# Kernel optimization log

Hardware: AMD Instinct MI355X
Metric: run time of the kernel (lower is better)

Reference implementation:

```python
import jax, jax.numpy as jnp
import numpy as np

B, S, DM = 2, 2048, 1024
H, D = 16, 64  # multiheads, head_dim; H*D == DM
NEG = -1e9


def setup_inputs() -> dict:
    key = jax.random.key(0)
    ks = jax.random.split(key, 7)
    xavier = float(np.sqrt(6.0 / (DM + H * D)))
    return {
        "Q": jax.random.normal(ks[0], (B, S, DM), dtype=jnp.float32),
        "K": jax.random.normal(ks[1], (B, S, DM), dtype=jnp.float32),
        "V": jax.random.normal(ks[2], (B, S, DM), dtype=jnp.float32),
        "V_len": jax.random.randint(ks[3], (B,), 0, S),
        "WQ": jax.random.uniform(ks[4], (DM, H * D), dtype=jnp.float32, minval=-xavier, maxval=xavier),
        "WK": jax.random.uniform(ks[5], (DM, H * D), dtype=jnp.float32, minval=-xavier, maxval=xavier),
        "WV": jax.random.uniform(ks[6], (DM, H * D), dtype=jnp.float32, minval=-xavier, maxval=xavier),
    }


def reference(Q, K, V, V_len, WQ, WK, WV):
    b, s, _ = Q.shape
    # project and split heads: [B,S,DM] -> [B,H,S,D]
    q = (Q @ WQ).reshape(b, s, H, D).transpose(0, 2, 1, 3)
    k = (K @ WK).reshape(b, s, H, D).transpose(0, 2, 1, 3)
    v = (V @ WV).reshape(b, s, H, D).transpose(0, 2, 1, 3)
    scores = jnp.einsum("bhqd,bhkd->bhqk", q, k) / jnp.sqrt(jnp.float32(D))
    # key padding mask: valid keys are positions < V_len[b]
    valid = jnp.arange(s)[None, :] < V_len[:, None]          # [B,S]
    scores = jnp.where(valid[:, None, None, :], scores, NEG)  # [B,H,Sq,Sk]
    attn = jax.nn.softmax(scores, axis=-1)
    out = jnp.einsum("bhqk,bhkd->bhqd", attn, v)
    return out.transpose(0, 2, 1, 3).reshape(b, s, H * D)
```

## Files before the change

kernel.cpp:

```cpp
#include <hip/hip_runtime.h>
#include <hip/hip_bf16.h>

#define NBATCH 2
#define SEQ 2048
#define DMODEL 1024
#define NHEAD 16
#define HDIM 64
#define ROWS (NBATCH*SEQ)

typedef __attribute__((ext_vector_type(8))) short bf16x8;
typedef __attribute__((ext_vector_type(4))) float f32x4;
typedef __attribute__((ext_vector_type(16))) float f32x16;

#define MFMA16 __builtin_amdgcn_mfma_f32_16x16x32_bf16
#define MFMA32 __builtin_amdgcn_mfma_f32_32x32x16_bf16

#define QSCALE 0.1803368801111204f
#define DEFER_THR 11.541560327111708f

static __device__ __forceinline__ unsigned short f2bf(float f) {
    unsigned int u = __float_as_uint(f);
    u += 0x7fffu + ((u >> 16) & 1u);
    return (unsigned short)(u >> 16);
}

static __device__ __forceinline__ unsigned cvtpk(float lo, float hi) {
    unsigned r;
    asm("v_cvt_pk_bf16_f32 %0, %1, %2" : "=v"(r) : "v"(lo), "v"(hi));
    return r;
}

static __device__ __forceinline__ void gld16(const unsigned short* g, unsigned short* l) {
    __builtin_amdgcn_global_load_lds(
        (const __attribute__((address_space(1))) unsigned int*)g,
        (__attribute__((address_space(3))) unsigned int*)l,
        16, 0, 0);
}

__global__ __launch_bounds__(256) void cvt_kernel(const float* __restrict__ Q, const float* __restrict__ K,
                                                  const float* __restrict__ V, const int* __restrict__ vlenp,
                                                  unsigned short* __restrict__ dq, unsigned short* __restrict__ dk,
                                                  unsigned short* __restrict__ dv, int n8) {
    int i = blockIdx.x * 256 + threadIdx.x;
    if (i >= n8) return;
    const int z = blockIdx.z;
    if (z) {
        int row = i >> 7;
        int bb = row >> 11, s = row & 2047;
        int vl = vlenp[bb];
        int lim = ((vl + 31) >> 5) << 5;
        if (z == 1) { if (vl == 0 || s >= lim) return; }
        else        { if (vl != 0 && s >= lim) return; }
    }
    const float* src = z == 0 ? Q : (z == 1 ? K : V);
    unsigned short* dst = z == 0 ? dq : (z == 1 ? dk : dv);
    const float4* s4 = (const float4*)src;
    float4 a = s4[2 * i], b = s4[2 * i + 1];
    union { bf16x8 v; unsigned short u[8]; } o;
    o.u[0] = f2bf(a.x); o.u[1] = f2bf(a.y); o.u[2] = f2bf(a.z); o.u[3] = f2bf(a.w);
    o.u[4] = f2bf(b.x); o.u[5] = f2bf(b.y); o.u[6] = f2bf(b.z); o.u[7] = f2bf(b.w);
    *(bf16x8*)(dst + (size_t)i * 8) = o.v;
}

__global__ __launch_bounds__(256) void wtrans_kernel(const float* __restrict__ W0, const float* __restrict__ W1,
                                                     const float* __restrict__ W2,
                                                     unsigned short* __restrict__ T0, unsigned short* __restrict__ T1,
                                                     unsigned short* __restrict__ T2) {
    const float* W = blockIdx.z == 0 ? W0 : (blockIdx.z == 1 ? W1 : W2);
    unsigned short* T = blockIdx.z == 0 ? T0 : (blockIdx.z == 1 ? T1 : T2);
    __shared__ float tile[64][65];
    int rb = blockIdx.y * 64, cb = blockIdx.x * 64;
    int tid = threadIdx.x;
    #pragma unroll
    for (int rep = 0; rep < 16; ++rep) {
        int idx = rep * 256 + tid; int r = idx >> 6, c = idx & 63;
        tile[r][c] = W[(size_t)(rb + r) * DMODEL + cb + c];
    }
    __syncthreads();
    #pragma unroll
    for (int rep = 0; rep < 16; ++rep) {
        int idx = rep * 256 + tid; int r = idx >> 6, c = idx & 63;
        T[(size_t)(cb + r) * DMODEL + rb + c] = f2bf(tile[c][r]);
    }
}

__global__ __launch_bounds__(256) void proj_kernel(
        const unsigned short* __restrict__ Xq, const unsigned short* __restrict__ Xk,
        const unsigned short* __restrict__ Xv,
        const unsigned short* __restrict__ WTq, const unsigned short* __restrict__ WTk,
        const unsigned short* __restrict__ WTv, const int* __restrict__ vlenp,
        unsigned short* __restrict__ qp, unsigned short* __restrict__ kp,
        unsigned short* __restrict__ vtp) {
    const int mode = blockIdx.z;
    {
    }
    const int lin = blockIdx.y * gridDim.x + blockIdx.x;
    const int xcd = lin & 7, chunk = lin >> 3;
    const int by2 = xcd * 4 + (chunk >> 3);
    const int bx2 = chunk & 7;
    const int rowBase = by2 * 128;
    const int colBase = bx2 * 128;

    if (mode >= 1) {
        const int bb = rowBase >> 11, sS = rowBase & 2047;
        const int vl = vlenp[bb];
        const int lim = ((vl + 31) >> 5) << 5;
        if (mode == 1) { if (vl == 0 || sS >= lim) return; }
        else           { if (vl != 0 && sS >= lim) return; }
    }

    const unsigned short* X  = mode == 0 ? Xq  : (mode == 1 ? Xk  : Xv);
    const unsigned short* WT = mode == 0 ? WTq : (mode == 1 ? WTk : WTv);

    __shared__ unsigned short As[2][128 * 64];
    __shared__ unsigned short Bs[2][128 * 64];

    const int tid = threadIdx.x, lane = tid & 63, w = tid >> 6;
    const int wr = w >> 1, wc = w & 1;

    const int Xwave = (mode < 2) ? wr : wc;
    const int Wwave = (mode < 2) ? wc : wr;

    const int rloc = lane >> 3;
    const int ssw  = ((lane & 7) * 8) ^ (rloc * 8);

    f32x4 acc[4][4];
    #pragma unroll
    for (int i = 0; i < 4; ++i)
        #pragma unroll
        for (int j = 0; j < 4; ++j) acc[i][j] = (f32x4){0.f, 0.f, 0.f, 0.f};

    auto stage = [&](int kt, int buf) {
        #pragma unroll
        for (int j = 0; j < 4; ++j) {
            int c = w * 4 + j;
            int r = c * 8 + rloc;
            gld16(X  + (size_t)(rowBase + r) * DMODEL + kt * 64 + ssw, &As[buf][c * 512]);
            gld16(WT + (size_t)(colBase + r) * DMODEL + kt * 64 + ssw, &Bs[buf][c * 512]);
        }
    };

    stage(0, 0);
    __syncthreads();

    for (int kt = 0; kt < DMODEL / 64; ++kt) {
        const int cur = kt & 1;
        if (kt + 1 < DMODEL / 64) stage(kt + 1, cur ^ 1);

        #pragma unroll
        for (int ks = 0; ks < 2; ++ks) {
            const int kbyte = ks * 64 + ((lane >> 4) * 16);
            bf16x8 xf[4], wf[4];
            #pragma unroll
            for (int i = 0; i < 4; ++i) {
                int xr = Xwave * 64 + i * 16 + (lane & 15);
                xf[i] = *(const bf16x8*)((const char*)&As[cur][0] + xr * 128 + (kbyte ^ ((xr & 7) << 4)));
                int wrow = Wwave * 64 + i * 16 + (lane & 15);
                wf[i] = *(const bf16x8*)((const char*)&Bs[cur][0] + wrow * 128 + (kbyte ^ ((wrow & 7) << 4)));
            }
            if (mode < 2) {
                #pragma unroll
                for (int i = 0; i < 4; ++i)
                    #pragma unroll
                    for (int j = 0; j < 4; ++j)
                        acc[i][j] = MFMA16(xf[i], wf[j], acc[i][j], 0, 0, 0);
            } else {
                #pragma unroll
                for (int i = 0; i < 4; ++i)
                    #pragma unroll
                    for (int j = 0; j < 4; ++j)
                        acc[i][j] = MFMA16(wf[i], xf[j], acc[i][j], 0, 0, 0);
            }
        }
        __syncthreads();
    }

    if (mode < 2) {
        unsigned short* outp = (mode == 0) ? qp : kp;
        const float sc = (mode == 0) ? QSCALE : 1.0f;
        #pragma unroll
        for (int i = 0; i < 4; ++i)
            #pragma unroll
            for (int j = 0; j < 4; ++j)
                #pragma unroll
                for (int r = 0; r < 4; ++r) {
                    int grow = rowBase + wr * 64 + i * 16 + (lane >> 4) * 4 + r;
                    int gcol = colBase + wc * 64 + j * 16 + (lane & 15);
                    int b = grow >> 11, s = grow & 2047, hh = gcol >> 6, d = gcol & 63;
                    outp[((size_t)(b * NHEAD + hh) * SEQ + s) * HDIM + d] = f2bf(acc[i][j][r] * sc);
                }
    } else {
        #pragma unroll
        for (int i = 0; i < 4; ++i)
            #pragma unroll
            for (int j = 0; j < 4; ++j)
                #pragma unroll
                for (int r = 0; r < 4; ++r) {
                    int gcol = colBase + wr * 64 + i * 16 + (lane >> 4) * 4 + r;
                    int grow = rowBase + wc * 64 + j * 16 + (lane & 15);
                    int b = grow >> 11, s = grow & 2047, hh = gcol >> 6, d = gcol & 63;
                    vtp[((size_t)(b * NHEAD + hh) * HDIM + d) * SEQ + s] = f2bf(acc[i][j][r]);
                }
    }
}

__global__ __launch_bounds__(256, 4) void attn_kernel(
        const unsigned short* __restrict__ qp, const unsigned short* __restrict__ kp,
        const unsigned short* __restrict__ vtp, const int* __restrict__ vlenp,
        float* __restrict__ out) {
    const int tid = threadIdx.x, lane = tid & 63, w = tid >> 6;
    const int hh = lane >> 5;
    const int ql = lane & 31;
    const int qsub = w >> 1, kpar = w & 1;
    const int qt = blockIdx.x, h = blockIdx.y, b = blockIdx.z;
    const int vlen = vlenp[b];
    const int nt = (vlen == 0) ? (SEQ / 32) : ((vlen + 31) >> 5);
    const int myn = (nt - kpar + 1) >> 1;
    const int J = (nt + 1) >> 1;

    __shared__ unsigned short Kd[2][2][2048];
    __shared__ unsigned short Vd[2][2][2048];
    __shared__ float mlb[4][2][32];

    const size_t headQ = (size_t)(b * NHEAD + h) * SEQ * HDIM;
    const size_t headV = (size_t)(b * NHEAD + h) * HDIM * SEQ;

    const int qrow = qt * 64 + qsub * 32 + ql;
    bf16x8 qf[4];
    #pragma unroll
    for (int ks = 0; ks < 4; ++ks)
        qf[ks] = *(const bf16x8*)(qp + headQ + (size_t)qrow * HDIM + ks * 16 + hh * 8);

    f32x16 o0, o1;
    #pragma unroll
    for (int r = 0; r < 16; ++r) { o0[r] = 0.f; o1[r] = 0.f; }
    float m_run = -1e30f, l_run = 0.f;

    const int rloc = lane >> 3;
    const int ssw  = ((lane & 7) * 8) ^ (rloc * 8);
    const int gn   = (lane & 7) ^ rloc;
    const int koff = (gn & 3) * 8;
    const int dhi  = (gn >> 2) * 32;

    auto stageK = [&](int kvB, int buf) {
        #pragma unroll
        for (int c = 0; c < 4; ++c)
            gld16(kp + headQ + (size_t)(kvB + c * 8 + rloc) * HDIM + ssw, &Kd[kpar][buf][c * 512]);
    };
    auto stageV = [&](int kvB, int buf) {
        #pragma unroll
        for (int c = 0; c < 4; ++c)
            gld16(vtp + headV + (size_t)(c * 8 + rloc + dhi) * SEQ + kvB + koff, &Vd[kpar][buf][c * 512]);
    };

    if (myn > 0) { if (qsub == 0) stageK(kpar * 32, 0); else stageV(kpar * 32, 0); }

    for (int j = 0; j < J; ++j) {
        const int cur = j & 1;
        __syncthreads();

        if (j + 1 < myn) {
            const int nb = (kpar + 2 * (j + 1)) * 32;
            if (qsub == 0) stageK(nb, cur ^ 1); else stageV(nb, cur ^ 1);
        }

        if (j < myn) {
            const int kvBase = (kpar + 2 * j) * 32;
            const char* Kb = (const char*)&Kd[kpar][cur][0];
            const char* Vb = (const char*)&Vd[kpar][cur][0];

            f32x16 s0;
            #pragma unroll
            for (int r = 0; r < 16; ++r) s0[r] = 0.f;
            __builtin_amdgcn_s_setprio(1);
            #pragma unroll
            for (int ks = 0; ks < 4; ++ks) {
                const int kb = (ks * 32 + hh * 16) ^ ((ql & 7) << 4);
                bf16x8 kf = *(const bf16x8*)(Kb + ql * 128 + kb);
                s0 = MFMA32(kf, qf[ks], s0, 0, 0, 0);
            }
            __builtin_amdgcn_s_setprio(0);

            if (kvBase + 32 > vlen) {
                #pragma unroll
                for (int r = 0; r < 16; ++r) {
                    int kl = (r & 3) + 8 * (r >> 2) + 4 * hh;
                    if (kvBase + kl >= vlen) s0[r] = -1e9f;
                }
            }

            float mx[8];
            #pragma unroll
            for (int t = 0; t < 8; ++t) mx[t] = fmaxf(s0[t], s0[t + 8]);
            #pragma unroll
            for (int st = 4; st > 0; st >>= 1)
                #pragma unroll
                for (int t = 0; t < st; ++t) mx[t] = fmaxf(mx[t], mx[t + st]);
            float tmax = fmaxf(mx[0], __shfl_xor(mx[0], 32));

            if (!__all(tmax <= m_run + DEFER_THR)) {
                const float mnew = fmaxf(m_run, tmax);
                const float al = __builtin_amdgcn_exp2f(m_run - mnew);
                l_run *= al;
                #pragma unroll
                for (int r = 0; r < 16; ++r) { o0[r] *= al; o1[r] *= al; }
                m_run = mnew;
            }

            #pragma unroll
            for (int r = 0; r < 16; ++r) s0[r] = __builtin_amdgcn_exp2f(s0[r] - m_run);
            float sm[8];
            #pragma unroll
            for (int t = 0; t < 8; ++t) sm[t] = s0[t] + s0[t + 8];
            #pragma unroll
            for (int st = 4; st > 0; st >>= 1)
                #pragma unroll
                for (int t = 0; t < st; ++t) sm[t] += sm[t + st];
            l_run += sm[0] + __shfl_xor(sm[0], 32);

            unsigned d0[8];
            #pragma unroll
            for (int t = 0; t < 8; ++t) d0[t] = cvtpk(s0[2 * t], s0[2 * t + 1]);

            __builtin_amdgcn_s_setprio(1);
#define PV_SLICE(KSL)                                                              \
            {                                                                      \
                unsigned a0 = d0[4 * (KSL)],     b0 = d0[4 * (KSL) + 2];           \
                unsigned a1 = d0[4 * (KSL) + 1], b1 = d0[4 * (KSL) + 3];           \
                asm("v_permlane32_swap_b32 %0, %1" : "+v"(a0), "+v"(b0));          \
                asm("v_permlane32_swap_b32 %0, %1" : "+v"(a1), "+v"(b1));          \
                union { unsigned u[4]; bf16x8 v; } pa;                             \
                pa.u[0] = a0; pa.u[1] = a1; pa.u[2] = b0; pa.u[3] = b1;            \
                const int gA = 2 * (KSL) + hh;                                     \
                bf16x8 vfA = *(const bf16x8*)(Vb + ql * 128 + ((gA ^ (ql & 7)) << 4));        \
                bf16x8 vfB = *(const bf16x8*)(Vb + ql * 128 + (((4 + gA) ^ (ql & 7)) << 4));  \
                o0 = MFMA32(vfA, pa.v, o0, 0, 0, 0);                               \
                o1 = MFMA32(vfB, pa.v, o1, 0, 0, 0);                               \
            }
            PV_SLICE(0)
            PV_SLICE(1)
#undef PV_SLICE
            __builtin_amdgcn_s_setprio(0);
        }
    }

    if (hh == 0) { mlb[w][0][ql] = m_run; mlb[w][1][ql] = l_run; }
    __syncthreads();
    if (kpar == 1) {
        char* Ob = ((char*)Kd) + qsub * 8192;
        #pragma unroll
        for (int g = 0; g < 4; ++g) {
            int ad = ql * 256 + ((32 * g + 16 * hh) ^ (16 * (ql & 7)));
            *(float4*)(Ob + ad)       = make_float4(o0[4*g], o0[4*g+1], o0[4*g+2], o0[4*g+3]);
            *(float4*)(Ob + ad + 128) = make_float4(o1[4*g], o1[4*g+1], o1[4*g+2], o1[4*g+3]);
        }
    }
    __syncthreads();
    if (kpar == 0) {
        const float mp = mlb[w + 1][0][ql], lp = mlb[w + 1][1][ql];
        const float M = fmaxf(m_run, mp);
        const float a0 = __builtin_amdgcn_exp2f(m_run - M);
        const float a1 = __builtin_amdgcn_exp2f(mp - M);
        const float linv = 1.0f / (l_run * a0 + lp * a1);
        const char* Pb = ((const char*)Kd) + qsub * 8192;
        float* orow = out + (size_t)(b * SEQ + qrow) * DMODEL + h * HDIM;
        #pragma unroll
        for (int g = 0; g < 4; ++g) {
            int ad = ql * 256 + ((32 * g + 16 * hh) ^ (16 * (ql & 7)));
            float4 p0 = *(const float4*)(Pb + ad);
            float4 p1 = *(const float4*)(Pb + ad + 128);
            *(float4*)(orow + 8 * g + 4 * hh) = make_float4(
                (o0[4*g]   * a0 + p0.x * a1) * linv, (o0[4*g+1] * a0 + p0.y * a1) * linv,
                (o0[4*g+2] * a0 + p0.z * a1) * linv, (o0[4*g+3] * a0 + p0.w * a1) * linv);
            *(float4*)(orow + 32 + 8 * g + 4 * hh) = make_float4(
                (o1[4*g]   * a0 + p1.x * a1) * linv, (o1[4*g+1] * a0 + p1.y * a1) * linv,
                (o1[4*g+2] * a0 + p1.z * a1) * linv, (o1[4*g+3] * a0 + p1.w * a1) * linv);
        }
    }
}

extern "C" void kernel_launch(void* const* d_in, const int* in_sizes, int n_in,
                              void* d_out, int out_size, void* d_ws, size_t ws_size,
                              hipStream_t stream) {
    const float* Q  = (const float*)d_in[0];
    const float* K  = (const float*)d_in[1];
    const float* V  = (const float*)d_in[2];
    const int* V_len = (const int*)d_in[3];
    const float* WQ = (const float*)d_in[4];
    const float* WK = (const float*)d_in[5];
    const float* WV = (const float*)d_in[6];
    float* out = (float*)d_out;

    char* ws = (char*)d_ws;
    const size_t MB = 1024 * 1024;
    unsigned short* Xq  = (unsigned short*)(ws + 0 * MB);
    unsigned short* Xk  = (unsigned short*)(ws + 8 * MB);
    unsigned short* Xv  = (unsigned short*)(ws + 16 * MB);
    unsigned short* WTq = (unsigned short*)(ws + 24 * MB);
    unsigned short* WTk = (unsigned short*)(ws + 26 * MB);
    unsigned short* WTv = (unsigned short*)(ws + 28 * MB);
    unsigned short* qpj = (unsigned short*)(ws + 30 * MB);
    unsigned short* kpj = (unsigned short*)(ws + 38 * MB);
    unsigned short* vtp = (unsigned short*)(ws + 46 * MB);

    const int n8 = ROWS * DMODEL / 8;
    cvt_kernel<<<dim3((n8 + 255) / 256, 1, 3), 256, 0, stream>>>(Q, K, V, V_len, Xq, Xk, Xv, n8);
    wtrans_kernel<<<dim3(16, 16, 3), 256, 0, stream>>>(WQ, WK, WV, WTq, WTk, WTv);
    proj_kernel<<<dim3(8, 32, 3), 256, 0, stream>>>(
        Xq, Xk, Xv, WTq, WTk, WTv, V_len, qpj, kpj, vtp);
    attn_kernel<<<dim3(SEQ / 64, NHEAD, NBATCH), 256, 0, stream>>>(qpj, kpj, vtp, V_len, out);
}
```

Before: 88.09 us.

## Fold weight transpose into convert kernel and use single-buffered 128-wide K tiles

The weight transpose/convert kernel is merged into the input convert kernel as an extra grid z-slice, which removes one kernel launch. The projection GEMM drops its double-buffered 64-wide K staging. It now loads 128-wide K tiles into a single LDS buffer, with a barrier before compute, so the main loop runs half as many iterations and barriers. The trade-off is that global-to-LDS loads no longer overlap MFMA compute, which may expose memory latency in the projection.

```diff
diff --git a/kernel.cpp b/kernel.cpp
--- a/kernel.cpp
+++ b/kernel.cpp
@@ -39,11 +39,37 @@
 
 __global__ __launch_bounds__(256) void cvt_kernel(const float* __restrict__ Q, const float* __restrict__ K,
                                                   const float* __restrict__ V, const int* __restrict__ vlenp,
+                                                  const float* __restrict__ W0, const float* __restrict__ W1,
+                                                  const float* __restrict__ W2,
                                                   unsigned short* __restrict__ dq, unsigned short* __restrict__ dk,
-                                                  unsigned short* __restrict__ dv, int n8) {
-    int i = blockIdx.x * 256 + threadIdx.x;
+                                                  unsigned short* __restrict__ dv,
+                                                  unsigned short* __restrict__ T0, unsigned short* __restrict__ T1,
+                                                  unsigned short* __restrict__ T2, int n8) {
+    __shared__ float tile[64][65];
+    const int z = blockIdx.z;
+    const int tid = threadIdx.x;
+    if (z == 3) {
+        const int bx = blockIdx.x;
+        if (bx >= 768) return;
+        const int mat = bx >> 8, idx = bx & 255;
+        const float* W = mat == 0 ? W0 : (mat == 1 ? W1 : W2);
+        unsigned short* T = mat == 0 ? T0 : (mat == 1 ? T1 : T2);
+        int rb = (idx >> 4) * 64, cb = (idx & 15) * 64;
+        #pragma unroll
+        for (int rep = 0; rep < 16; ++rep) {
+            int i = rep * 256 + tid; int r = i >> 6, c = i & 63;
+            tile[r][c] = W[(size_t)(rb + r) * DMODEL + cb + c];
+        }
+        __syncthreads();
+        #pragma unroll
+        for (int rep = 0; rep < 16; ++rep) {
+            int i = rep * 256 + tid; int r = i >> 6, c = i & 63;
+            T[(size_t)(cb + r) * DMODEL + rb + c] = f2bf(tile[c][r]);
+        }
+        return;
+    }
+    int i = blockIdx.x * 256 + tid;
     if (i >= n8) return;
-    const int z = blockIdx.z;
     if (z) {
         int row = i >> 7;
         int bb = row >> 11, s = row & 2047;
@@ -62,28 +88,6 @@
     *(bf16x8*)(dst + (size_t)i * 8) = o.v;
 }
 
-__global__ __launch_bounds__(256) void wtrans_kernel(const float* __restrict__ W0, const float* __restrict__ W1,
-                                                     const float* __restrict__ W2,
-                                                     unsigned short* __restrict__ T0, unsigned short* __restrict__ T1,
-                                                     unsigned short* __restrict__ T2) {
-    const float* W = blockIdx.z == 0 ? W0 : (blockIdx.z == 1 ? W1 : W2);
-    unsigned short* T = blockIdx.z == 0 ? T0 : (blockIdx.z == 1 ? T1 : T2);
-    __shared__ float tile[64][65];
-    int rb = blockIdx.y * 64, cb = blockIdx.x * 64;
-    int tid = threadIdx.x;
-    #pragma unroll
-    for (int rep = 0; rep < 16; ++rep) {
-        int idx = rep * 256 + tid; int r = idx >> 6, c = idx & 63;
-        tile[r][c] = W[(size_t)(rb + r) * DMODEL + cb + c];
-    }
-    __syncthreads();
-    #pragma unroll
-    for (int rep = 0; rep < 16; ++rep) {
-        int idx = rep * 256 + tid; int r = idx >> 6, c = idx & 63;
-        T[(size_t)(cb + r) * DMODEL + rb + c] = f2bf(tile[c][r]);
-    }
-}
-
 __global__ __launch_bounds__(256) void proj_kernel(
         const unsigned short* __restrict__ Xq, const unsigned short* __restrict__ Xk,
         const unsigned short* __restrict__ Xv,
@@ -92,8 +96,6 @@
         unsigned short* __restrict__ qp, unsigned short* __restrict__ kp,
         unsigned short* __restrict__ vtp) {
     const int mode = blockIdx.z;
-    {
-    }
     const int lin = blockIdx.y * gridDim.x + blockIdx.x;
     const int xcd = lin & 7, chunk = lin >> 3;
     const int by2 = xcd * 4 + (chunk >> 3);
@@ -112,17 +114,14 @@
     const unsigned short* X  = mode == 0 ? Xq  : (mode == 1 ? Xk  : Xv);
     const unsigned short* WT = mode == 0 ? WTq : (mode == 1 ? WTk : WTv);
 
-    __shared__ unsigned short As[2][128 * 64];
-    __shared__ unsigned short Bs[2][128 * 64];
+    __shared__ unsigned short As[128 * 128];
+    __shared__ unsigned short Bs[128 * 128];
 
     const int tid = threadIdx.x, lane = tid & 63, w = tid >> 6;
     const int wr = w >> 1, wc = w & 1;
 
     const int Xwave = (mode < 2) ? wr : wc;
     const int Wwave = (mode < 2) ? wc : wr;
-
-    const int rloc = lane >> 3;
-    const int ssw  = ((lane & 7) * 8) ^ (rloc * 8);
 
     f32x4 acc[4][4];
     #pragma unroll
@@ -130,33 +129,29 @@
         #pragma unroll
         for (int j = 0; j < 4; ++j) acc[i][j] = (f32x4){0.f, 0.f, 0.f, 0.f};
 
-    auto stage = [&](int kt, int buf) {
-        #pragma unroll
-        for (int j = 0; j < 4; ++j) {
-            int c = w * 4 + j;
-            int r = c * 8 + rloc;
-            gld16(X  + (size_t)(rowBase + r) * DMODEL + kt * 64 + ssw, &As[buf][c * 512]);
-            gld16(WT + (size_t)(colBase + r) * DMODEL + kt * 64 + ssw, &Bs[buf][c * 512]);
-        }
-    };
-
-    stage(0, 0);
-    __syncthreads();
-
-    for (int kt = 0; kt < DMODEL / 64; ++kt) {
-        const int cur = kt & 1;
-        if (kt + 1 < DMODEL / 64) stage(kt + 1, cur ^ 1);
-
-        #pragma unroll
-        for (int ks = 0; ks < 2; ++ks) {
-            const int kbyte = ks * 64 + ((lane >> 4) * 16);
+    const int rl4 = lane >> 4;
+    const int gl  = lane & 15;
+
+    for (int kt = 0; kt < DMODEL / 128; ++kt) {
+        #pragma unroll
+        for (int j = 0; j < 8; ++j) {
+            int c = w * 8 + j;
+            int r = c * 4 + rl4;
+            int gg = gl ^ (r & 7);
+            gld16(X  + (size_t)(rowBase + r) * DMODEL + kt * 128 + gg * 8, &As[c * 512]);
+            gld16(WT + (size_t)(colBase + r) * DMODEL + kt * 128 + gg * 8, &Bs[c * 512]);
+        }
+        __syncthreads();
+        #pragma unroll
+        for (int ks = 0; ks < 4; ++ks) {
+            const int kbyteNom = ks * 64 + ((lane >> 4) * 16);
             bf16x8 xf[4], wf[4];
             #pragma unroll
             for (int i = 0; i < 4; ++i) {
                 int xr = Xwave * 64 + i * 16 + (lane & 15);
-                xf[i] = *(const bf16x8*)((const char*)&As[cur][0] + xr * 128 + (kbyte ^ ((xr & 7) << 4)));
+                xf[i] = *(const bf16x8*)((const char*)As + xr * 256 + (kbyteNom ^ ((xr & 7) << 4)));
                 int wrow = Wwave * 64 + i * 16 + (lane & 15);
-                wf[i] = *(const bf16x8*)((const char*)&Bs[cur][0] + wrow * 128 + (kbyte ^ ((wrow & 7) << 4)));
+                wf[i] = *(const bf16x8*)((const char*)Bs + wrow * 256 + (kbyteNom ^ ((wrow & 7) << 4)));
             }
             if (mode < 2) {
                 #pragma unroll
@@ -404,8 +399,8 @@
     unsigned short* vtp = (unsigned short*)(ws + 46 * MB);
 
     const int n8 = ROWS * DMODEL / 8;
-    cvt_kernel<<<dim3((n8 + 255) / 256, 1, 3), 256, 0, stream>>>(Q, K, V, V_len, Xq, Xk, Xv, n8);
-    wtrans_kernel<<<dim3(16, 16, 3), 256, 0, stream>>>(WQ, WK, WV, WTq, WTk, WTv);
+    cvt_kernel<<<dim3((n8 + 255) / 256, 1, 4), 256, 0, stream>>>(
+        Q, K, V, V_len, WQ, WK, WV, Xq, Xk, Xv, WTq, WTk, WTv, n8);
     proj_kernel<<<dim3(8, 32, 3), 256, 0, stream>>>(
         Xq, Xk, Xv, WTq, WTk, WTv, V_len, qpj, kpj, vtp);
     attn_kernel<<<dim3(SEQ / 64, NHEAD, NBATCH), 256, 0, stream>>>(qpj, kpj, vtp, V_len, out);
```

Measured after the change: 84.37 us. 4.2% less time.

## Fuse fp32-to-bf16 input conversion into projection GEMM and drop cvt kernel

Applied to the files above, without the earlier changes.

Removes the separate conversion kernel. The projection GEMM now loads fp32 activations directly, converts them to bf16 in registers and writes them swizzled into shared memory. This avoids a full write and re-read of bf16 copies of Q, K and V plus one launch. In exchange the K loop becomes single-buffered over 128-wide steps, losing the earlier async double-buffered prefetch, and it reads twice the bytes per activation tile. It also remaps the block-to-XCD row ordering and flattens the weight transpose grid.

```diff
diff --git a/kernel.cpp b/kernel.cpp
--- a/kernel.cpp
+++ b/kernel.cpp
@@ -37,66 +37,40 @@
         16, 0, 0);
 }
 
-__global__ __launch_bounds__(256) void cvt_kernel(const float* __restrict__ Q, const float* __restrict__ K,
-                                                  const float* __restrict__ V, const int* __restrict__ vlenp,
-                                                  unsigned short* __restrict__ dq, unsigned short* __restrict__ dk,
-                                                  unsigned short* __restrict__ dv, int n8) {
-    int i = blockIdx.x * 256 + threadIdx.x;
-    if (i >= n8) return;
-    const int z = blockIdx.z;
-    if (z) {
-        int row = i >> 7;
-        int bb = row >> 11, s = row & 2047;
-        int vl = vlenp[bb];
-        int lim = ((vl + 31) >> 5) << 5;
-        if (z == 1) { if (vl == 0 || s >= lim) return; }
-        else        { if (vl != 0 && s >= lim) return; }
-    }
-    const float* src = z == 0 ? Q : (z == 1 ? K : V);
-    unsigned short* dst = z == 0 ? dq : (z == 1 ? dk : dv);
-    const float4* s4 = (const float4*)src;
-    float4 a = s4[2 * i], b = s4[2 * i + 1];
-    union { bf16x8 v; unsigned short u[8]; } o;
-    o.u[0] = f2bf(a.x); o.u[1] = f2bf(a.y); o.u[2] = f2bf(a.z); o.u[3] = f2bf(a.w);
-    o.u[4] = f2bf(b.x); o.u[5] = f2bf(b.y); o.u[6] = f2bf(b.z); o.u[7] = f2bf(b.w);
-    *(bf16x8*)(dst + (size_t)i * 8) = o.v;
-}
-
 __global__ __launch_bounds__(256) void wtrans_kernel(const float* __restrict__ W0, const float* __restrict__ W1,
                                                      const float* __restrict__ W2,
                                                      unsigned short* __restrict__ T0, unsigned short* __restrict__ T1,
                                                      unsigned short* __restrict__ T2) {
-    const float* W = blockIdx.z == 0 ? W0 : (blockIdx.z == 1 ? W1 : W2);
-    unsigned short* T = blockIdx.z == 0 ? T0 : (blockIdx.z == 1 ? T1 : T2);
     __shared__ float tile[64][65];
-    int rb = blockIdx.y * 64, cb = blockIdx.x * 64;
-    int tid = threadIdx.x;
+    const int bx = blockIdx.x;
+    const int mat = bx >> 8, idx = bx & 255;
+    const float* W = mat == 0 ? W0 : (mat == 1 ? W1 : W2);
+    unsigned short* T = mat == 0 ? T0 : (mat == 1 ? T1 : T2);
+    const int rb = (idx >> 4) * 64, cb = (idx & 15) * 64;
+    const int tid = threadIdx.x;
     #pragma unroll
     for (int rep = 0; rep < 16; ++rep) {
-        int idx = rep * 256 + tid; int r = idx >> 6, c = idx & 63;
+        int i = rep * 256 + tid; int r = i >> 6, c = i & 63;
         tile[r][c] = W[(size_t)(rb + r) * DMODEL + cb + c];
     }
     __syncthreads();
     #pragma unroll
     for (int rep = 0; rep < 16; ++rep) {
-        int idx = rep * 256 + tid; int r = idx >> 6, c = idx & 63;
+        int i = rep * 256 + tid; int r = i >> 6, c = i & 63;
         T[(size_t)(cb + r) * DMODEL + rb + c] = f2bf(tile[c][r]);
     }
 }
 
 __global__ __launch_bounds__(256) void proj_kernel(
-        const unsigned short* __restrict__ Xq, const unsigned short* __restrict__ Xk,
-        const unsigned short* __restrict__ Xv,
+        const float* __restrict__ Xq, const float* __restrict__ Xk, const float* __restrict__ Xv,
         const unsigned short* __restrict__ WTq, const unsigned short* __restrict__ WTk,
         const unsigned short* __restrict__ WTv, const int* __restrict__ vlenp,
         unsigned short* __restrict__ qp, unsigned short* __restrict__ kp,
         unsigned short* __restrict__ vtp) {
     const int mode = blockIdx.z;
-    {
-    }
     const int lin = blockIdx.y * gridDim.x + blockIdx.x;
     const int xcd = lin & 7, chunk = lin >> 3;
-    const int by2 = xcd * 4 + (chunk >> 3);
+    const int by2 = (chunk >> 3) * 8 + xcd;
     const int bx2 = chunk & 7;
     const int rowBase = by2 * 128;
     const int colBase = bx2 * 128;
@@ -109,7 +83,7 @@
         else           { if (vl != 0 && sS >= lim) return; }
     }
 
-    const unsigned short* X  = mode == 0 ? Xq  : (mode == 1 ? Xk  : Xv);
+    const float* X = mode == 0 ? Xq : (mode == 1 ? Xk : Xv);
     const unsigned short* WT = mode == 0 ? WTq : (mode == 1 ? WTk : WTv);
 
     __shared__ unsigned short As[2][128 * 64];
@@ -117,12 +91,12 @@
 
     const int tid = threadIdx.x, lane = tid & 63, w = tid >> 6;
     const int wr = w >> 1, wc = w & 1;
-
     const int Xwave = (mode < 2) ? wr : wc;
     const int Wwave = (mode < 2) ? wc : wr;
 
     const int rloc = lane >> 3;
-    const int ssw  = ((lane & 7) * 8) ^ (rloc * 8);
+    const int gl8  = lane & 7;
+    const int ssw  = (gl8 * 8) ^ (rloc * 8);
 
     f32x4 acc[4][4];
     #pragma unroll
@@ -130,48 +104,58 @@
         #pragma unroll
         for (int j = 0; j < 4; ++j) acc[i][j] = (f32x4){0.f, 0.f, 0.f, 0.f};
 
-    auto stage = [&](int kt, int buf) {
+    for (int kt = 0; kt < DMODEL / 128; ++kt) {
+        #pragma unroll
+        for (int hf = 0; hf < 2; ++hf)
+            #pragma unroll
+            for (int j = 0; j < 4; ++j) {
+                int c = w * 4 + j;
+                int r = c * 8 + rloc;
+                gld16(WT + (size_t)(colBase + r) * DMODEL + kt * 128 + hf * 64 + ssw, &Bs[hf][c * 512]);
+            }
         #pragma unroll
         for (int j = 0; j < 4; ++j) {
-            int c = w * 4 + j;
-            int r = c * 8 + rloc;
-            gld16(X  + (size_t)(rowBase + r) * DMODEL + kt * 64 + ssw, &As[buf][c * 512]);
-            gld16(WT + (size_t)(colBase + r) * DMODEL + kt * 64 + ssw, &Bs[buf][c * 512]);
-        }
-    };
-
-    stage(0, 0);
-    __syncthreads();
-
-    for (int kt = 0; kt < DMODEL / 64; ++kt) {
-        const int cur = kt & 1;
-        if (kt + 1 < DMODEL / 64) stage(kt + 1, cur ^ 1);
-
-        #pragma unroll
-        for (int ks = 0; ks < 2; ++ks) {
-            const int kbyte = ks * 64 + ((lane >> 4) * 16);
-            bf16x8 xf[4], wf[4];
-            #pragma unroll
-            for (int i = 0; i < 4; ++i) {
-                int xr = Xwave * 64 + i * 16 + (lane & 15);
-                xf[i] = *(const bf16x8*)((const char*)&As[cur][0] + xr * 128 + (kbyte ^ ((xr & 7) << 4)));
-                int wrow = Wwave * 64 + i * 16 + (lane & 15);
-                wf[i] = *(const bf16x8*)((const char*)&Bs[cur][0] + wrow * 128 + (kbyte ^ ((wrow & 7) << 4)));
-            }
-            if (mode < 2) {
-                #pragma unroll
-                for (int i = 0; i < 4; ++i)
+            const int r = (w * 4 + j) * 8 + rloc;
+            const float* rowp = X + (size_t)(rowBase + r) * DMODEL + kt * 128 + gl8 * 8;
+            #pragma unroll
+            for (int hf = 0; hf < 2; ++hf) {
+                float4 f0 = *(const float4*)(rowp + hf * 64);
+                float4 f1 = *(const float4*)(rowp + hf * 64 + 4);
+                union { unsigned short u[8]; int4 v; } t;
+                t.u[0] = f2bf(f0.x); t.u[1] = f2bf(f0.y); t.u[2] = f2bf(f0.z); t.u[3] = f2bf(f0.w);
+                t.u[4] = f2bf(f1.x); t.u[5] = f2bf(f1.y); t.u[6] = f2bf(f1.z); t.u[7] = f2bf(f1.w);
+                *(int4*)(&As[hf][r * 64 + ((gl8 ^ (r & 7)) * 8)]) = t.v;
+            }
+        }
+        __syncthreads();
+
+        #pragma unroll
+        for (int hf = 0; hf < 2; ++hf)
+            #pragma unroll
+            for (int ks = 0; ks < 2; ++ks) {
+                const int kbyte = ks * 64 + ((lane >> 4) * 16);
+                bf16x8 xf[4], wf[4];
+                #pragma unroll
+                for (int i = 0; i < 4; ++i) {
+                    int xr = Xwave * 64 + i * 16 + (lane & 15);
+                    xf[i] = *(const bf16x8*)((const char*)&As[hf][0] + xr * 128 + (kbyte ^ ((xr & 7) << 4)));
+                    int wrow = Wwave * 64 + i * 16 + (lane & 15);
+                    wf[i] = *(const bf16x8*)((const char*)&Bs[hf][0] + wrow * 128 + (kbyte ^ ((wrow & 7) << 4)));
+                }
+                if (mode < 2) {
                     #pragma unroll
-                    for (int j = 0; j < 4; ++j)
-                        acc[i][j] = MFMA16(xf[i], wf[j], acc[i][j], 0, 0, 0);
-            } else {
-                #pragma unroll
-                for (int i = 0; i < 4; ++i)
+                    for (int i = 0; i < 4; ++i)
+                        #pragma unroll
+                        for (int j = 0; j < 4; ++j)
+                            acc[i][j] = MFMA16(xf[i], wf[j], acc[i][j], 0, 0, 0);
+                } else {
                     #pragma unroll
-                    for (int j = 0; j < 4; ++j)
-                        acc[i][j] = MFMA16(wf[i], xf[j], acc[i][j], 0, 0, 0);
-            }
-        }
+                    for (int i = 0; i < 4; ++i)
+                        #pragma unroll
+                        for (int j = 0; j < 4; ++j)
+                            acc[i][j] = MFMA16(wf[i], xf[j], acc[i][j], 0, 0, 0);
+                }
+            }
         __syncthreads();
     }
 
@@ -393,9 +377,6 @@
 
     char* ws = (char*)d_ws;
     const size_t MB = 1024 * 1024;
-    unsigned short* Xq  = (unsigned short*)(ws + 0 * MB);
-    unsigned short* Xk  = (unsigned short*)(ws + 8 * MB);
-    unsigned short* Xv  = (unsigned short*)(ws + 16 * MB);
     unsigned short* WTq = (unsigned short*)(ws + 24 * MB);
     unsigned short* WTk = (unsigned short*)(ws + 26 * MB);
     unsigned short* WTv = (unsigned short*)(ws + 28 * MB);
@@ -403,10 +384,8 @@
     unsigned short* kpj = (unsigned short*)(ws + 38 * MB);
     unsigned short* vtp = (unsigned short*)(ws + 46 * MB);
 
-    const int n8 = ROWS * DMODEL / 8;
-    cvt_kernel<<<dim3((n8 + 255) / 256, 1, 3), 256, 0, stream>>>(Q, K, V, V_len, Xq, Xk, Xv, n8);
-    wtrans_kernel<<<dim3(16, 16, 3), 256, 0, stream>>>(WQ, WK, WV, WTq, WTk, WTv);
+    wtrans_kernel<<<dim3(768), 256, 0, stream>>>(WQ, WK, WV, WTq, WTk, WTv);
     proj_kernel<<<dim3(8, 32, 3), 256, 0, stream>>>(
-        Xq, Xk, Xv, WTq, WTk, WTv, V_len, qpj, kpj, vtp);
+        Q, K, V, WTq, WTk, WTv, V_len, qpj, kpj, vtp);
     attn_kernel<<<dim3(SEQ / 64, NHEAD, NBATCH), 256, 0, stream>>>(qpj, kpj, vtp, V_len, out);
 }
```

New measurement: 88.38 us. No clear change (+0.3%).
